# Kernel tuning notes

Hardware: AMD Instinct MI355X
Metric: run time of the kernel (lower is better)

The kernel has to match this reference:

```python
import jax, jax.numpy as jnp
import numpy as np

N_NODES = 100000
N_EDGES = 3200000
F_IN = 16
H1 = 50
H2 = 20


def gcn_conv(x, W, b, src, dst, ew, n):
    """GCNConv with add_self_loops=True and symmetric normalization."""
    xw = x @ W  # [n, out]  (transform first: out < in traffic)
    loop = jnp.arange(n, dtype=src.dtype)
    src_f = jnp.concatenate([src, loop])
    dst_f = jnp.concatenate([dst, loop])
    ew_f = jnp.concatenate([ew, jnp.ones((n,), ew.dtype)])
    deg = jax.ops.segment_sum(ew_f, dst_f, num_segments=n)
    dinv = jnp.where(deg > 0, jax.lax.rsqrt(deg), 0.0)
    norm = dinv[src_f] * ew_f * dinv[dst_f]  # [E+n]
    agg = jax.ops.segment_sum(norm[:, None] * xw[src_f], dst_f, num_segments=n)
    return agg + b


def tgcn_cell(x, H, src, dst, ew, n, p):
    # p: dict of params for one TGCN cell
    cz = gcn_conv(x, p['wz'], p['bz'], src, dst, ew, n)
    Z = jax.nn.sigmoid(jnp.concatenate([cz, H], axis=1) @ p['lz_w'].T + p['lz_b'])
    cr = gcn_conv(x, p['wr'], p['br'], src, dst, ew, n)
    R = jax.nn.sigmoid(jnp.concatenate([cr, H], axis=1) @ p['lr_w'].T + p['lr_b'])
    ch = gcn_conv(x, p['wh'], p['bh'], src, dst, ew, n)
    Ht = jnp.tanh(jnp.concatenate([ch, H * R], axis=1) @ p['lh_w'].T + p['lh_b'])
    return Z * H + (1.0 - Z) * Ht


def _cell_params(key, fin, fout):
    ks = jax.random.split(key, 6)
    s_c = 1.0 / np.sqrt(fin)
    s_l = 1.0 / np.sqrt(2 * fout)
    names = ['z', 'r', 'h']
    p = {}
    for i, nm in enumerate(names):
        p['w' + nm] = jax.random.normal(ks[2 * i], (fin, fout), jnp.float32) * s_c
        p['b' + nm] = jnp.zeros((fout,), jnp.float32)
        p['l' + nm + '_w'] = jax.random.normal(ks[2 * i + 1], (fout, 2 * fout), jnp.float32) * s_l
        p['l' + nm + '_b'] = jnp.zeros((fout,), jnp.float32)
    return p


def setup_inputs() -> dict:
    key = jax.random.key(0)
    k = jax.random.split(key, 6)
    x = jax.random.normal(k[0], (N_NODES, F_IN), jnp.float32)
    edge_index = jax.random.randint(k[1], (2, N_EDGES), 0, N_NODES, jnp.int32)
    edge_weight = jax.random.uniform(k[2], (N_EDGES,), jnp.float32)
    p1 = _cell_params(k[3], F_IN, H1)
    p2 = _cell_params(k[4], H1, H2)
    inp = {'x': x, 'edge_index': edge_index, 'edge_weight': edge_weight}
    for nm, v in p1.items():
        inp['c1_' + nm] = v
    for nm, v in p2.items():
        inp['c2_' + nm] = v
    inp['lin_w'] = jax.random.normal(k[5], (1, H2), jnp.float32) * (1.0 / np.sqrt(H2))
    inp['lin_b'] = jnp.zeros((1,), jnp.float32)
    return inp


def reference(x, edge_index, edge_weight,
              c1_wz, c1_bz, c1_lz_w, c1_lz_b, c1_wr, c1_br, c1_lr_w, c1_lr_b,
              c1_wh, c1_bh, c1_lh_w, c1_lh_b,
              c2_wz, c2_bz, c2_lz_w, c2_lz_b, c2_wr, c2_br, c2_lr_w, c2_lr_b,
              c2_wh, c2_bh, c2_lh_w, c2_lh_b,
              lin_w, lin_b):
    n = x.shape[0]
    src, dst = edge_index[0], edge_index[1]
    p1 = dict(wz=c1_wz, bz=c1_bz, lz_w=c1_lz_w, lz_b=c1_lz_b,
              wr=c1_wr, br=c1_br, lr_w=c1_lr_w, lr_b=c1_lr_b,
              wh=c1_wh, bh=c1_bh, lh_w=c1_lh_w, lh_b=c1_lh_b)
    p2 = dict(wz=c2_wz, bz=c2_bz, lz_w=c2_lz_w, lz_b=c2_lz_b,
              wr=c2_wr, br=c2_br, lr_w=c2_lr_w, lr_b=c2_lr_b,
              wh=c2_wh, bh=c2_bh, lh_w=c2_lh_w, lh_b=c2_lh_b)
    h = tgcn_cell(x, jnp.zeros((n, H1), x.dtype), src, dst, edge_weight, n, p1)
    h = jax.nn.relu(h)  # dropout is identity in eval mode
    h = tgcn_cell(h, jnp.zeros((n, H2), x.dtype), src, dst, edge_weight, n, p2)
    h = jax.nn.relu(h)
    return h @ lin_w.T + lin_b  # [n, 1]
```

## Files before the change

### kernel.cpp

```cpp
#include <hip/hip_runtime.h>
#include <math.h>

#define N_NODES 100000
#define N_EDGES 3200000
#define F_IN 16
#define H1 50
#define H2 20
#define C1 100
#define C2 40
#define STRIDE 72
#define NB 391
#define BCAP 9216
#define EPT_A 16

__global__ void k_binA(const int* __restrict__ dst, const int* __restrict__ src,
                       const float* __restrict__ ew, int* __restrict__ gcur,
                       int2* __restrict__ ebuf) {
    __shared__ int cnt[NB];
    __shared__ int base[NB];
    int tid = threadIdx.x;
    for (int b = tid; b < NB; b += 256) cnt[b] = 0;
    __syncthreads();
    int e0 = blockIdx.x * (256 * EPT_A);
    unsigned meta[EPT_A], ewb[EPT_A];
    int bb[EPT_A], rr[EPT_A];
#pragma unroll
    for (int i = 0; i < EPT_A; ++i) {
        int e = e0 + i * 256 + tid;
        bool v = (e < N_EDGES);
        int d = v ? dst[e] : 0;
        int s = v ? src[e] : 0;
        float w = v ? ew[e] : 0.f;
        int b = d >> 8;
        int r = 0;
        if (v) r = atomicAdd(&cnt[b], 1);
        meta[i] = (unsigned)s | ((unsigned)(d & 255) << 17);
        ewb[i]  = __float_as_uint(w);
        bb[i]   = v ? b : -1;
        rr[i]   = r;
    }
    __syncthreads();
    for (int b = tid; b < NB; b += 256) {
        int c = cnt[b];
        base[b] = c ? atomicAdd(&gcur[b], c) : 0;
    }
    __syncthreads();
#pragma unroll
    for (int i = 0; i < EPT_A; ++i) {
        if (bb[i] >= 0) {
            int p = base[bb[i]] + rr[i];
            if (p < BCAP)
                ebuf[(size_t)bb[i] * BCAP + p] = make_int2((int)meta[i], (int)ewb[i]);
        }
    }
}

__global__ void k_binB(const int* __restrict__ gcur, const int2* __restrict__ ebuf,
                       int* __restrict__ cur, float* __restrict__ dinv,
                       int2* __restrict__ se) {
    __shared__ int   lcur[256];
    __shared__ float ldeg[256];
    int tid = threadIdx.x;
    int b   = blockIdx.x;
    if (tid < 256) { lcur[tid] = 0; ldeg[tid] = 0.f; }
    __syncthreads();
    int nE = min(gcur[b], BCAP);
    const int2* eb = ebuf + (size_t)b * BCAP;
    for (int i = tid; i < nE; i += 512) {
        int2 rec = eb[i];
        unsigned m = (unsigned)rec.x;
        int dlow = (int)(m >> 17);
        int s    = (int)(m & 0x1FFFFu);
        int r = atomicAdd(&lcur[dlow], 1);
        int node = (b << 8) + dlow;
        if (r < STRIDE)
            se[(size_t)node * STRIDE + r] = make_int2(s, rec.y);
        atomicAdd(&ldeg[dlow], __uint_as_float((unsigned)rec.y));
    }
    __syncthreads();
    if (tid < 256) {
        int node = (b << 8) + tid;
        if (node < N_NODES) {
            cur[node]  = node * STRIDE + min(lcur[tid], STRIDE);
            dinv[node] = rsqrtf(ldeg[tid] + 1.0f);
        }
    }
}

__global__ void k_y(const float* __restrict__ x, const float* __restrict__ dinv,
                    float* __restrict__ y) {
    int t = blockIdx.x * blockDim.x + threadIdx.x;
    int i = t >> 3, j = t & 7;
    if (i >= N_NODES) return;
    float2 v = ((const float2*)x)[(unsigned)i * 8 + j];
    float di = dinv[i];
    v.x *= di; v.y *= di;
    ((float2*)y)[(unsigned)i * 8 + j] = v;
}

__global__ void k_gather1(const int* __restrict__ cur, const int2* __restrict__ se,
                          const float* __restrict__ y, float* __restrict__ g) {
    int t = blockIdx.x * blockDim.x + threadIdx.x;
    int node = t >> 3, j = t & 7;
    if (node >= N_NODES) return;
    int beg = node * STRIDE;
    int end = min(cur[node], beg + STRIDE);
    const float2* y2 = (const float2*)y;
    float2 a0 = {0.f, 0.f}, a1 = {0.f, 0.f}, a2 = {0.f, 0.f}, a3 = {0.f, 0.f};
    int k = beg;
    for (; k + 4 <= end; k += 4) {
        int2 p0 = se[k], p1 = se[k + 1], p2 = se[k + 2], p3 = se[k + 3];
        float2 v0 = y2[(unsigned)p0.x * 8 + j];
        float2 v1 = y2[(unsigned)p1.x * 8 + j];
        float2 v2 = y2[(unsigned)p2.x * 8 + j];
        float2 v3 = y2[(unsigned)p3.x * 8 + j];
        float w0 = __int_as_float(p0.y), w1 = __int_as_float(p1.y);
        float w2 = __int_as_float(p2.y), w3 = __int_as_float(p3.y);
        a0.x = fmaf(w0, v0.x, a0.x); a0.y = fmaf(w0, v0.y, a0.y);
        a1.x = fmaf(w1, v1.x, a1.x); a1.y = fmaf(w1, v1.y, a1.y);
        a2.x = fmaf(w2, v2.x, a2.x); a2.y = fmaf(w2, v2.y, a2.y);
        a3.x = fmaf(w3, v3.x, a3.x); a3.y = fmaf(w3, v3.y, a3.y);
    }
    for (; k < end; ++k) {
        int2 p = se[k];
        float2 v = y2[(unsigned)p.x * 8 + j];
        float w = __int_as_float(p.y);
        a0.x = fmaf(w, v.x, a0.x); a0.y = fmaf(w, v.y, a0.y);
    }
    float2 r;
    r.x = (a0.x + a1.x) + (a2.x + a3.x);
    r.y = (a0.y + a1.y) + (a2.y + a3.y);
    ((float2*)g)[(unsigned)node * 8 + j] = r;
}

__global__ void k_conv1_gate_xs2(const float* __restrict__ g, const float* __restrict__ x,
                                 const float* __restrict__ dinv,
                                 const float* __restrict__ wz, const float* __restrict__ wh,
                                 const float* __restrict__ cbz, const float* __restrict__ cbh,
                                 const float* __restrict__ lzw, const float* __restrict__ lzb,
                                 const float* __restrict__ lhw, const float* __restrict__ lhb,
                                 const float* __restrict__ w2z, const float* __restrict__ w2h,
                                 float* __restrict__ xs2) {
    __shared__ float wcat[F_IN][C1];
    __shared__ float zw[H1][H1 + 1];
    __shared__ float hw[H1][H1 + 1];
    __shared__ float w2[H1][C2];
    __shared__ float zb[H1], hb[H1];
    __shared__ float tv[4][F_IN];
    __shared__ float cz[4][H1], ch[4][H1], hr[4][H1];
    int tid = threadIdx.x;
    for (int t = tid; t < F_IN * H1; t += 256) {
        int k = t / H1, jj = t % H1;
        wcat[k][jj]      = wz[t];
        wcat[k][H1 + jj] = wh[t];
    }
    for (int t = tid; t < H1 * H1; t += 256) {
        int j = t / H1, k = t % H1;
        zw[j][k] = lzw[j * (2 * H1) + k];
        hw[j][k] = lhw[j * (2 * H1) + k];
    }
    for (int t = tid; t < H1 * H2; t += 256) {
        int k = t / H2, j = t % H2;
        w2[k][j]      = w2z[t];
        w2[k][H2 + j] = w2h[t];
    }
    if (tid < H1) { zb[tid] = lzb[tid]; hb[tid] = lhb[tid]; }
    int nl = tid >> 6, j = tid & 63;
    int i  = blockIdx.x * 4 + nl;
    bool valid = (i < N_NODES);
    float di = valid ? dinv[i] : 0.f;
    if (valid && j < F_IN)
        tv[nl][j] = g[(unsigned)i * F_IN + j] + di * x[(unsigned)i * F_IN + j];
    __syncthreads();
    if (valid && j < H1) {
        float az = 0.f, ah = 0.f;
#pragma unroll
        for (int k = 0; k < F_IN; ++k) {
            float t = tv[nl][k];
            az = fmaf(t, wcat[k][j],      az);
            ah = fmaf(t, wcat[k][H1 + j], ah);
        }
        cz[nl][j] = di * az + cbz[j];
        ch[nl][j] = di * ah + cbh[j];
    }
    __syncthreads();
    if (valid && j < H1) {
        float az = zb[j], ah = hb[j];
#pragma unroll 10
        for (int k = 0; k < H1; ++k) {
            az = fmaf(cz[nl][k], zw[j][k], az);
            ah = fmaf(ch[nl][k], hw[j][k], ah);
        }
        float Z = 1.f / (1.f + expf(-az));
        hr[nl][j] = fmaxf((1.f - Z) * tanhf(ah), 0.f);
    }
    __syncthreads();
    if (valid && j < C2) {
        float a = 0.f;
#pragma unroll 10
        for (int k = 0; k < H1; ++k) a = fmaf(hr[nl][k], w2[k][j], a);
        xs2[(unsigned)i * C2 + j] = di * a;
    }
}

__global__ void k_gather2(const int* __restrict__ cur, const int2* __restrict__ se,
                          const float* __restrict__ xs, float* __restrict__ acc) {
    int tid  = threadIdx.x;
    int node = blockIdx.x * 16 + tid / 20;
    unsigned j = (unsigned)(tid % 20);
    if (node >= N_NODES) return;
    int beg = node * STRIDE;
    int end = min(cur[node], beg + STRIDE);
    const float2* x2 = (const float2*)xs;
    float2 a0 = {0.f, 0.f}, a1 = {0.f, 0.f}, a2 = {0.f, 0.f}, a3 = {0.f, 0.f};
    int k = beg;
    for (; k + 4 <= end; k += 4) {
        int2 p0 = se[k], p1 = se[k + 1], p2 = se[k + 2], p3 = se[k + 3];
        float2 v0 = x2[(unsigned)p0.x * 20 + j];
        float2 v1 = x2[(unsigned)p1.x * 20 + j];
        float2 v2 = x2[(unsigned)p2.x * 20 + j];
        float2 v3 = x2[(unsigned)p3.x * 20 + j];
        float w0 = __int_as_float(p0.y), w1 = __int_as_float(p1.y);
        float w2 = __int_as_float(p2.y), w3 = __int_as_float(p3.y);
        a0.x = fmaf(w0, v0.x, a0.x); a0.y = fmaf(w0, v0.y, a0.y);
        a1.x = fmaf(w1, v1.x, a1.x); a1.y = fmaf(w1, v1.y, a1.y);
        a2.x = fmaf(w2, v2.x, a2.x); a2.y = fmaf(w2, v2.y, a2.y);
        a3.x = fmaf(w3, v3.x, a3.x); a3.y = fmaf(w3, v3.y, a3.y);
    }
    for (; k < end; ++k) {
        int2 p = se[k];
        float2 v = x2[(unsigned)p.x * 20 + j];
        float w = __int_as_float(p.y);
        a0.x = fmaf(w, v.x, a0.x); a0.y = fmaf(w, v.y, a0.y);
    }
    float2 r;
    r.x = (a0.x + a1.x) + (a2.x + a3.x);
    r.y = (a0.y + a1.y) + (a2.y + a3.y);
    ((float2*)acc)[(unsigned)node * 20 + j] = r;
}

__global__ void k_cell2_gate_out(const float* __restrict__ acc2, const float* __restrict__ xs2,
                                 const float* __restrict__ dinv,
                                 const float* __restrict__ cbz, const float* __restrict__ cbh,
                                 const float* __restrict__ lzw, const float* __restrict__ lzb,
                                 const float* __restrict__ lhw, const float* __restrict__ lhb,
                                 const float* __restrict__ linw, const float* __restrict__ linb,
                                 float* __restrict__ out) {
    __shared__ float zw[H2][H2], hw[H2][H2];
    __shared__ float zb[H2], hb[H2], lw[H2];
    __shared__ float rowbuf[64][C2 + 1];
    int tid = threadIdx.x;
    for (int t = tid; t < H2 * H2; t += 64) {
        int j = t / H2, k = t % H2;
        zw[j][k] = lzw[j * (2 * H2) + k];
        hw[j][k] = lhw[j * (2 * H2) + k];
    }
    if (tid < H2) { zb[tid] = lzb[tid]; hb[tid] = lhb[tid]; lw[tid] = linw[tid]; }
    int base = blockIdx.x * 64;
    for (int t = tid; t < 64 * C2; t += 64) {
        int il = t / C2, k = t % C2;
        size_t idx = (size_t)(base + il) * C2 + k;
        if (base + il < N_NODES) rowbuf[il][k] = acc2[idx] + xs2[idx];
    }
    __syncthreads();
    int i = base + tid;
    if (i >= N_NODES) return;
    float di = dinv[i];
    float czv[H2], chv[H2];
#pragma unroll
    for (int k = 0; k < H2; ++k) {
        czv[k] = di * rowbuf[tid][k]      + cbz[k];
        chv[k] = di * rowbuf[tid][H2 + k] + cbh[k];
    }
    float o = 0.f;
    for (int j = 0; j < H2; ++j) {
        float az = zb[j], ah = hb[j];
#pragma unroll
        for (int k = 0; k < H2; ++k) {
            az = fmaf(czv[k], zw[j][k], az);
            ah = fmaf(chv[k], hw[j][k], ah);
        }
        float Z  = 1.f / (1.f + expf(-az));
        float Ht = tanhf(ah);
        o = fmaf(fmaxf((1.f - Z) * Ht, 0.f), lw[j], o);
    }
    out[i] = o + linb[0];
}

extern "C" void kernel_launch(void* const* d_in, const int* in_sizes, int n_in,
                              void* d_out, int out_size, void* d_ws, size_t ws_size,
                              hipStream_t stream) {
    const float* x      = (const float*)d_in[0];
    const int*   ei     = (const int*)d_in[1];
    const int*   src    = ei;
    const int*   dst    = ei + N_EDGES;
    const float* ew     = (const float*)d_in[2];
    const float* c1_wz  = (const float*)d_in[3];
    const float* c1_bz  = (const float*)d_in[4];
    const float* c1_lzw = (const float*)d_in[5];
    const float* c1_lzb = (const float*)d_in[6];
    const float* c1_wh  = (const float*)d_in[11];
    const float* c1_bh  = (const float*)d_in[12];
    const float* c1_lhw = (const float*)d_in[13];
    const float* c1_lhb = (const float*)d_in[14];
    const float* c2_wz  = (const float*)d_in[15];
    const float* c2_bz  = (const float*)d_in[16];
    const float* c2_lzw = (const float*)d_in[17];
    const float* c2_lzb = (const float*)d_in[18];
    const float* c2_wh  = (const float*)d_in[23];
    const float* c2_bh  = (const float*)d_in[24];
    const float* c2_lhw = (const float*)d_in[25];
    const float* c2_lhb = (const float*)d_in[26];
    const float* linw   = (const float*)d_in[27];
    const float* linb   = (const float*)d_in[28];
    float* out = (float*)d_out;

    int*   cur  = (int*)d_ws;
    float* dinv = (float*)(cur + N_NODES);
    int*   gcur = (int*)(dinv + N_NODES);
    int2*  se   = (int2*)(gcur + 512);
    float* xs2  = (float*)(se + (size_t)N_NODES * STRIDE);
    float* y    = xs2 + (size_t)N_NODES * C2;
    float* g    = y + (size_t)N_NODES * F_IN;
    float* acc2 = y;
    int2*  ebuf = (int2*)xs2;

    hipMemsetAsync(gcur, 0, NB * sizeof(int), stream);
    k_binA<<<(N_EDGES + 256 * EPT_A - 1) / (256 * EPT_A), 256, 0, stream>>>(
        dst, src, ew, gcur, ebuf);
    k_binB<<<NB, 512, 0, stream>>>(gcur, ebuf, cur, dinv, se);
    k_y<<<(N_NODES * 8 + 255) / 256, 256, 0, stream>>>(x, dinv, y);

    k_gather1<<<(N_NODES * 8 + 255) / 256, 256, 0, stream>>>(cur, se, y, g);
    k_conv1_gate_xs2<<<(N_NODES + 3) / 4, 256, 0, stream>>>(g, x, dinv,
        c1_wz, c1_wh, c1_bz, c1_bh, c1_lzw, c1_lzb, c1_lhw, c1_lhb,
        c2_wz, c2_wh, xs2);

    k_gather2<<<(N_NODES + 15) / 16, 320, 0, stream>>>(cur, se, xs2, acc2);
    k_cell2_gate_out<<<(N_NODES + 63) / 64, 64, 0, stream>>>(acc2, xs2, dinv,
        c2_bz, c2_bh, c2_lzw, c2_lzb, c2_lhw, c2_lhb, linw, linb, out);
}
```

Before: 557.9 us.

## Amortize shared weight staging over 64 nodes per block in conv1 gate kernel

Each block of k_conv1_gate_xs2 now loops over 16 groups of 4 nodes, 64 in total, instead of handling only 4. The many-kilobyte shared-memory weight load is therefore paid once per 64 nodes rather than once per 4. The next group's g/x/dinv values are prefetched into registers, and expf/tanhf are replaced with __expf-based forms in both gate kernels. The trade-offs are a grid 16x smaller, an extra barrier per iteration, and slightly lower transcendental accuracy.

```diff
diff --git a/kernel.cpp b/kernel.cpp
--- a/kernel.cpp
+++ b/kernel.cpp
@@ -12,6 +12,7 @@
 #define NB 391
 #define BCAP 9216
 #define EPT_A 16
+#define NPB 64
 
 __global__ void k_binA(const int* __restrict__ dst, const int* __restrict__ src,
                        const float* __restrict__ ew, int* __restrict__ gcur,
@@ -133,21 +134,22 @@
     ((float2*)g)[(unsigned)node * 8 + j] = r;
 }
 
-__global__ void k_conv1_gate_xs2(const float* __restrict__ g, const float* __restrict__ x,
-                                 const float* __restrict__ dinv,
-                                 const float* __restrict__ wz, const float* __restrict__ wh,
-                                 const float* __restrict__ cbz, const float* __restrict__ cbh,
-                                 const float* __restrict__ lzw, const float* __restrict__ lzb,
-                                 const float* __restrict__ lhw, const float* __restrict__ lhb,
-                                 const float* __restrict__ w2z, const float* __restrict__ w2h,
-                                 float* __restrict__ xs2) {
+__global__ __launch_bounds__(256) void k_conv1_gate_xs2(
+        const float* __restrict__ g, const float* __restrict__ x,
+        const float* __restrict__ dinv,
+        const float* __restrict__ wz, const float* __restrict__ wh,
+        const float* __restrict__ cbz, const float* __restrict__ cbh,
+        const float* __restrict__ lzw, const float* __restrict__ lzb,
+        const float* __restrict__ lhw, const float* __restrict__ lhb,
+        const float* __restrict__ w2z, const float* __restrict__ w2h,
+        float* __restrict__ xs2) {
     __shared__ float wcat[F_IN][C1];
-    __shared__ float zw[H1][H1 + 1];
-    __shared__ float hw[H1][H1 + 1];
+    __shared__ float zw[H1][52];
+    __shared__ float hw[H1][52];
     __shared__ float w2[H1][C2];
-    __shared__ float zb[H1], hb[H1];
+    __shared__ float czb[H1], chb[H1], zbb[H1], hbb[H1];
     __shared__ float tv[4][F_IN];
-    __shared__ float cz[4][H1], ch[4][H1], hr[4][H1];
+    __shared__ float cz[4][52], ch[4][52], hr[4][52];
     int tid = threadIdx.x;
     for (int t = tid; t < F_IN * H1; t += 256) {
         int k = t / H1, jj = t % H1;
@@ -164,42 +166,61 @@
         w2[k][j]      = w2z[t];
         w2[k][H2 + j] = w2h[t];
     }
-    if (tid < H1) { zb[tid] = lzb[tid]; hb[tid] = lhb[tid]; }
-    int nl = tid >> 6, j = tid & 63;
-    int i  = blockIdx.x * 4 + nl;
-    bool valid = (i < N_NODES);
-    float di = valid ? dinv[i] : 0.f;
-    if (valid && j < F_IN)
-        tv[nl][j] = g[(unsigned)i * F_IN + j] + di * x[(unsigned)i * F_IN + j];
-    __syncthreads();
-    if (valid && j < H1) {
-        float az = 0.f, ah = 0.f;
-#pragma unroll
-        for (int k = 0; k < F_IN; ++k) {
-            float t = tv[nl][k];
-            az = fmaf(t, wcat[k][j],      az);
-            ah = fmaf(t, wcat[k][H1 + j], ah);
-        }
-        cz[nl][j] = di * az + cbz[j];
-        ch[nl][j] = di * ah + cbh[j];
-    }
-    __syncthreads();
-    if (valid && j < H1) {
-        float az = zb[j], ah = hb[j];
+    if (tid < H1) {
+        czb[tid] = cbz[tid]; chb[tid] = cbh[tid];
+        zbb[tid] = lzb[tid]; hbb[tid] = lhb[tid];
+    }
+    __syncthreads();
+
+    int wid = tid >> 6, lane = tid & 63;
+    int i = blockIdx.x * NPB + wid;
+    float pg = 0.f, px = 0.f, pdi = 0.f;
+    if (i < N_NODES) {
+        pdi = dinv[i];
+        if (lane < F_IN) { pg = g[(unsigned)i * F_IN + lane]; px = x[(unsigned)i * F_IN + lane]; }
+    }
+    for (int it = 0; it < NPB / 4; ++it) {
+        int icur = i;
+        float di = pdi, gv = pg, xv = px;
+        i += 4;
+        if (it + 1 < NPB / 4 && i < N_NODES) {
+            pdi = dinv[i];
+            if (lane < F_IN) { pg = g[(unsigned)i * F_IN + lane]; px = x[(unsigned)i * F_IN + lane]; }
+        }
+        bool valid = (icur < N_NODES);
+        if (valid && lane < F_IN) tv[wid][lane] = gv + di * xv;
+        __syncthreads();
+        if (valid && lane < H1) {
+            float az = 0.f, ah = 0.f;
+#pragma unroll
+            for (int k = 0; k < F_IN; ++k) {
+                float t = tv[wid][k];
+                az = fmaf(t, wcat[k][lane],      az);
+                ah = fmaf(t, wcat[k][H1 + lane], ah);
+            }
+            cz[wid][lane] = di * az + czb[lane];
+            ch[wid][lane] = di * ah + chb[lane];
+        }
+        __syncthreads();
+        if (valid && lane < H1) {
+            float az = zbb[lane], ah = hbb[lane];
 #pragma unroll 10
-        for (int k = 0; k < H1; ++k) {
-            az = fmaf(cz[nl][k], zw[j][k], az);
-            ah = fmaf(ch[nl][k], hw[j][k], ah);
-        }
-        float Z = 1.f / (1.f + expf(-az));
-        hr[nl][j] = fmaxf((1.f - Z) * tanhf(ah), 0.f);
-    }
-    __syncthreads();
-    if (valid && j < C2) {
-        float a = 0.f;
+            for (int k = 0; k < H1; ++k) {
+                az = fmaf(cz[wid][k], zw[lane][k], az);
+                ah = fmaf(ch[wid][k], hw[lane][k], ah);
+            }
+            float Z  = 1.f / (1.f + __expf(-az));
+            float Ht = 1.f - 2.f / (__expf(2.f * ah) + 1.f);
+            hr[wid][lane] = fmaxf((1.f - Z) * Ht, 0.f);
+        }
+        __syncthreads();
+        if (valid && lane < C2) {
+            float a = 0.f;
 #pragma unroll 10
-        for (int k = 0; k < H1; ++k) a = fmaf(hr[nl][k], w2[k][j], a);
-        xs2[(unsigned)i * C2 + j] = di * a;
+            for (int k = 0; k < H1; ++k) a = fmaf(hr[wid][k], w2[k][lane], a);
+            xs2[(unsigned)icur * C2 + lane] = di * a;
+        }
+        __syncthreads();
     }
 }
 
@@ -280,8 +301,8 @@
             az = fmaf(czv[k], zw[j][k], az);
             ah = fmaf(chv[k], hw[j][k], ah);
         }
-        float Z  = 1.f / (1.f + expf(-az));
-        float Ht = tanhf(ah);
+        float Z  = 1.f / (1.f + __expf(-az));
+        float Ht = 1.f - 2.f / (__expf(2.f * ah) + 1.f);
         o = fmaf(fmaxf((1.f - Z) * Ht, 0.f), lw[j], o);
     }
     out[i] = o + linb[0];
@@ -332,7 +353,7 @@
     k_y<<<(N_NODES * 8 + 255) / 256, 256, 0, stream>>>(x, dinv, y);
 
     k_gather1<<<(N_NODES * 8 + 255) / 256, 256, 0, stream>>>(cur, se, y, g);
-    k_conv1_gate_xs2<<<(N_NODES + 3) / 4, 256, 0, stream>>>(g, x, dinv,
+    k_conv1_gate_xs2<<<(N_NODES + NPB - 1) / NPB, 256, 0, stream>>>(g, x, dinv,
         c1_wz, c1_wh, c1_bz, c1_bh, c1_lzw, c1_lzb, c1_lhw, c1_lhb,
         c2_wz, c2_wh, xs2);
 
```

New measurement: 544.1 us. 1.03x faster.

## Compute conv1 gate per thread-per-node and use fast exp/tanh intrinsics

Applied to the files above, without the earlier changes.

The layer-1 gate kernel changes from four nodes per 256-thread block, which staged all weight matrices into shared memory on every block, to one node per thread. Each thread keeps its intermediate vectors in registers and reads the weights directly from global memory, where every thread loads the same address. This removes the per-block weight staging, the barriers and the idle lanes, and adds vectorized float4 loads and stores. The cost is much higher register pressure (about 140 floats live per thread) and possible spills, and the fast __expf-based sigmoid and tanh in both gate kernels slightly change the numerics.

```diff
diff --git a/kernel.cpp b/kernel.cpp
--- a/kernel.cpp
+++ b/kernel.cpp
@@ -133,73 +133,74 @@
     ((float2*)g)[(unsigned)node * 8 + j] = r;
 }
 
-__global__ void k_conv1_gate_xs2(const float* __restrict__ g, const float* __restrict__ x,
-                                 const float* __restrict__ dinv,
-                                 const float* __restrict__ wz, const float* __restrict__ wh,
-                                 const float* __restrict__ cbz, const float* __restrict__ cbh,
-                                 const float* __restrict__ lzw, const float* __restrict__ lzb,
-                                 const float* __restrict__ lhw, const float* __restrict__ lhb,
-                                 const float* __restrict__ w2z, const float* __restrict__ w2h,
-                                 float* __restrict__ xs2) {
-    __shared__ float wcat[F_IN][C1];
-    __shared__ float zw[H1][H1 + 1];
-    __shared__ float hw[H1][H1 + 1];
-    __shared__ float w2[H1][C2];
-    __shared__ float zb[H1], hb[H1];
-    __shared__ float tv[4][F_IN];
-    __shared__ float cz[4][H1], ch[4][H1], hr[4][H1];
-    int tid = threadIdx.x;
-    for (int t = tid; t < F_IN * H1; t += 256) {
-        int k = t / H1, jj = t % H1;
-        wcat[k][jj]      = wz[t];
-        wcat[k][H1 + jj] = wh[t];
-    }
-    for (int t = tid; t < H1 * H1; t += 256) {
-        int j = t / H1, k = t % H1;
-        zw[j][k] = lzw[j * (2 * H1) + k];
-        hw[j][k] = lhw[j * (2 * H1) + k];
-    }
-    for (int t = tid; t < H1 * H2; t += 256) {
-        int k = t / H2, j = t % H2;
-        w2[k][j]      = w2z[t];
-        w2[k][H2 + j] = w2h[t];
-    }
-    if (tid < H1) { zb[tid] = lzb[tid]; hb[tid] = lhb[tid]; }
-    int nl = tid >> 6, j = tid & 63;
-    int i  = blockIdx.x * 4 + nl;
-    bool valid = (i < N_NODES);
-    float di = valid ? dinv[i] : 0.f;
-    if (valid && j < F_IN)
-        tv[nl][j] = g[(unsigned)i * F_IN + j] + di * x[(unsigned)i * F_IN + j];
-    __syncthreads();
-    if (valid && j < H1) {
+__global__ __launch_bounds__(256) void k_conv1_gate_xs2(
+        const float* __restrict__ g, const float* __restrict__ x,
+        const float* __restrict__ dinv,
+        const float* __restrict__ wz, const float* __restrict__ wh,
+        const float* __restrict__ cbz, const float* __restrict__ cbh,
+        const float* __restrict__ lzw, const float* __restrict__ lzb,
+        const float* __restrict__ lhw, const float* __restrict__ lhb,
+        const float* __restrict__ w2z, const float* __restrict__ w2h,
+        float* __restrict__ xs2) {
+    int i = blockIdx.x * blockDim.x + threadIdx.x;
+    if (i >= N_NODES) return;
+    float di = dinv[i];
+
+    float tv[F_IN];
+    const float4* g4 = (const float4*)(g + (size_t)i * F_IN);
+    const float4* x4 = (const float4*)(x + (size_t)i * F_IN);
+#pragma unroll
+    for (int q = 0; q < F_IN / 4; ++q) {
+        float4 gv = g4[q], xv = x4[q];
+        tv[4 * q + 0] = fmaf(di, xv.x, gv.x);
+        tv[4 * q + 1] = fmaf(di, xv.y, gv.y);
+        tv[4 * q + 2] = fmaf(di, xv.z, gv.z);
+        tv[4 * q + 3] = fmaf(di, xv.w, gv.w);
+    }
+
+    float cz[H1], ch[H1];
+#pragma unroll
+    for (int j = 0; j < H1; ++j) {
         float az = 0.f, ah = 0.f;
 #pragma unroll
         for (int k = 0; k < F_IN; ++k) {
-            float t = tv[nl][k];
-            az = fmaf(t, wcat[k][j],      az);
-            ah = fmaf(t, wcat[k][H1 + j], ah);
-        }
-        cz[nl][j] = di * az + cbz[j];
-        ch[nl][j] = di * ah + cbh[j];
-    }
-    __syncthreads();
-    if (valid && j < H1) {
-        float az = zb[j], ah = hb[j];
-#pragma unroll 10
+            az = fmaf(tv[k], wz[k * H1 + j], az);
+            ah = fmaf(tv[k], wh[k * H1 + j], ah);
+        }
+        cz[j] = fmaf(di, az, cbz[j]);
+        ch[j] = fmaf(di, ah, cbh[j]);
+    }
+
+    float acc[C2];
+#pragma unroll
+    for (int c = 0; c < C2; ++c) acc[c] = 0.f;
+    for (int j = 0; j < H1; ++j) {
+        const float* zr = lzw + j * (2 * H1);
+        const float* hrw = lhw + j * (2 * H1);
+        float az = lzb[j], ah = lhb[j];
+#pragma unroll
         for (int k = 0; k < H1; ++k) {
-            az = fmaf(cz[nl][k], zw[j][k], az);
-            ah = fmaf(ch[nl][k], hw[j][k], ah);
-        }
-        float Z = 1.f / (1.f + expf(-az));
-        hr[nl][j] = fmaxf((1.f - Z) * tanhf(ah), 0.f);
-    }
-    __syncthreads();
-    if (valid && j < C2) {
-        float a = 0.f;
-#pragma unroll 10
-        for (int k = 0; k < H1; ++k) a = fmaf(hr[nl][k], w2[k][j], a);
-        xs2[(unsigned)i * C2 + j] = di * a;
+            az = fmaf(cz[k], zr[k], az);
+            ah = fmaf(ch[k], hrw[k], ah);
+        }
+        float Z   = 1.f / (1.f + __expf(-az));
+        float Ht  = 1.f - 2.f / (__expf(2.f * ah) + 1.f);
+        float hrj = fmaxf((1.f - Z) * Ht, 0.f);
+        const float* w2zr = w2z + j * H2;
+        const float* w2hr = w2h + j * H2;
+#pragma unroll
+        for (int c = 0; c < H2; ++c) {
+            acc[c]      = fmaf(hrj, w2zr[c], acc[c]);
+            acc[H2 + c] = fmaf(hrj, w2hr[c], acc[H2 + c]);
+        }
+    }
+    float4* o4 = (float4*)(xs2 + (size_t)i * C2);
+#pragma unroll
+    for (int q = 0; q < C2 / 4; ++q) {
+        float4 v;
+        v.x = di * acc[4 * q + 0]; v.y = di * acc[4 * q + 1];
+        v.z = di * acc[4 * q + 2]; v.w = di * acc[4 * q + 3];
+        o4[q] = v;
     }
 }
 
@@ -280,8 +281,8 @@
             az = fmaf(czv[k], zw[j][k], az);
             ah = fmaf(chv[k], hw[j][k], ah);
         }
-        float Z  = 1.f / (1.f + expf(-az));
-        float Ht = tanhf(ah);
+        float Z  = 1.f / (1.f + __expf(-az));
+        float Ht = 1.f - 2.f / (__expf(2.f * ah) + 1.f);
         o = fmaf(fmaxf((1.f - Z) * Ht, 0.f), lw[j], o);
     }
     out[i] = o + linb[0];
@@ -332,7 +333,7 @@
     k_y<<<(N_NODES * 8 + 255) / 256, 256, 0, stream>>>(x, dinv, y);
 
     k_gather1<<<(N_NODES * 8 + 255) / 256, 256, 0, stream>>>(cur, se, y, g);
-    k_conv1_gate_xs2<<<(N_NODES + 3) / 4, 256, 0, stream>>>(g, x, dinv,
+    k_conv1_gate_xs2<<<(N_NODES + 255) / 256, 256, 0, stream>>>(g, x, dinv,
         c1_wz, c1_wh, c1_bz, c1_bh, c1_lzw, c1_lzb, c1_lhw, c1_lhb,
         c2_wz, c2_wh, xs2);
 
```

Measured after the change: 447.4 us. 19.8% less time.
